# Optimization experiments

Measured on AMD Instinct MI355X. Metric: run time of the kernel, lower is better.

## Reference

```python
import jax, jax.numpy as jnp
import numpy as np

N, M, C = 262144, 1048576, 32768
ORIG, AF, NF, GH, H, NG = 200, 64, 32, 16, 128, 3


def setup_inputs() -> dict:
    key = jax.random.key(0)
    ks = jax.random.split(key, 16)
    w = lambda k, s: (jax.random.normal(k, s) * 0.02).astype(jnp.float32)
    d = {}
    d["atom_weights"] = jax.random.uniform(ks[0], (N, 1), dtype=jnp.float32)
    d["orig_atom_fea"] = jax.random.normal(ks[1], (N, ORIG), dtype=jnp.float32)
    d["nbr_fea"] = jax.random.normal(ks[2], (M, NF), dtype=jnp.float32)
    d["self_fea_idx"] = jax.random.randint(ks[3], (M,), 0, N)
    d["nbr_fea_idx"] = jax.random.randint(ks[4], (M,), 0, N)
    d["crystal_atom_idx"] = jnp.sort(jax.random.randint(ks[5], (N,), 0, C))
    d["emb_W"] = w(ks[6], (ORIG, AF)); d["emb_b"] = jnp.zeros((AF,), jnp.float32)
    d["filt_W"] = w(ks[7], (NG, 2 * AF + NF, AF)); d["filt_b"] = jnp.zeros((NG, AF), jnp.float32)
    d["core_W"] = w(ks[8], (NG, 2 * AF + NF, AF)); d["core_b"] = jnp.zeros((NG, AF), jnp.float32)
    d["bn_f_g"] = jnp.ones((NG, AF), jnp.float32); d["bn_f_b"] = jnp.zeros((NG, AF), jnp.float32)
    d["bn_c_g"] = jnp.ones((NG, AF), jnp.float32); d["bn_c_b"] = jnp.zeros((NG, AF), jnp.float32)
    d["bn_o_g"] = jnp.ones((NG, AF), jnp.float32); d["bn_o_b"] = jnp.zeros((NG, AF), jnp.float32)
    d["gate_W1"] = w(ks[9], (AF, GH)); d["gate_b1"] = jnp.zeros((GH,), jnp.float32)
    d["gate_bn_g"] = jnp.ones((GH,), jnp.float32); d["gate_bn_b"] = jnp.zeros((GH,), jnp.float32)
    d["gate_W2"] = w(ks[10], (GH, 1)); d["gate_b2"] = jnp.zeros((1,), jnp.float32)
    d["fc_W"] = w(ks[11], (AF, H)); d["fc_b"] = jnp.zeros((H,), jnp.float32)
    d["fc_bn_g"] = jnp.ones((H,), jnp.float32); d["fc_bn_b"] = jnp.zeros((H,), jnp.float32)
    d["out_W"] = w(ks[12], (H, 1)); d["out_b"] = jnp.zeros((1,), jnp.float32)
    return d


def _bn(x, g, b, eps=1e-5):
    # training-mode BatchNorm1d: batch stats over dim 0, biased variance
    return (x - x.mean(0)) / jnp.sqrt(x.var(0) + eps) * g + b


def reference(atom_weights, orig_atom_fea, nbr_fea, self_fea_idx, nbr_fea_idx, crystal_atom_idx,
              emb_W, emb_b, filt_W, filt_b, core_W, core_b,
              bn_f_g, bn_f_b, bn_c_g, bn_c_b, bn_o_g, bn_o_b,
              gate_W1, gate_b1, gate_bn_g, gate_bn_b, gate_W2, gate_b2,
              fc_W, fc_b, fc_bn_g, fc_bn_b, out_W, out_b):
    atom = orig_atom_fea @ emb_W + emb_b  # (N, AF)
    cnt = jnp.clip(jax.ops.segment_sum(jnp.ones((M,), atom.dtype), self_fea_idx, N), 1.0)
    for i in range(NG):  # message-passing layers
        total = jnp.concatenate([atom[self_fea_idx], atom[nbr_fea_idx], nbr_fea], axis=1)  # (M, 2AF+NF)
        f = jax.nn.sigmoid(_bn(total @ filt_W[i] + filt_b[i], bn_f_g[i], bn_f_b[i]))
        c = jax.nn.softplus(_bn(total @ core_W[i] + core_b[i], bn_c_g[i], bn_c_b[i]))
        mean = jax.ops.segment_sum(f * c, self_fea_idx, N) / cnt[:, None]  # scatter_mean
        atom = jax.nn.softplus(atom + _bn(mean, bn_o_g[i], bn_o_b[i]))
    # GlobalAttention pooling over crystals
    gate = jax.nn.relu(_bn(atom @ gate_W1 + gate_b1, gate_bn_g, gate_bn_b)) @ gate_W2 + gate_b2  # (N,1)
    gmax = jax.ops.segment_max(gate, crystal_atom_idx, C)
    gate = atom_weights * jnp.exp(gate - gmax[crystal_atom_idx])
    gate = gate / (jax.ops.segment_sum(gate, crystal_atom_idx, C)[crystal_atom_idx] + 1e-13)
    crys = jax.ops.segment_sum(gate * atom, crystal_atom_idx, C)  # (C, AF)
    crys = jax.nn.softplus(_bn(crys @ fc_W + fc_b, fc_bn_g, fc_bn_b))
    return crys @ out_W + out_b  # (C, 1)
```

## Files before the change

### kernel.cpp

```cpp
#include <hip/hip_runtime.h>
#include <cstdint>
#include <cstddef>

#define NATOM 262144
#define MEDGE 1048576
#define NCRY  32768

typedef __attribute__((ext_vector_type(8))) short short8v;
typedef __attribute__((ext_vector_type(4))) float f32x4;

__device__ __forceinline__ float4 ld4(const float* p){ return *reinterpret_cast<const float4*>(p); }

__device__ __forceinline__ float softplusf_(float x){
  return fmaxf(x, 0.0f) + log1pf(expf(-fabsf(x)));
}
__device__ __forceinline__ float softplus_fast(float x){
  return fmaxf(x, 0.0f) + __logf(1.0f + __expf(-fabsf(x)));
}
__device__ __forceinline__ float sigmoid_fast(float y){
  return __builtin_amdgcn_rcpf(1.0f + __expf(-y));
}

__device__ __forceinline__ unsigned short rne_bf16(float f){
  unsigned u = __float_as_uint(f);
  unsigned r = u + 0x7FFFu + ((u >> 16) & 1u);
  return (unsigned short)(r >> 16);
}
__device__ __forceinline__ float bfu(short s){
  return __uint_as_float(((unsigned)(unsigned short)s) << 16);
}

__device__ __forceinline__ unsigned fkey(float x){
  unsigned b = __float_as_uint(x);
  return (b & 0x80000000u) ? ~b : (b | 0x80000000u);
}
__device__ __forceinline__ float fkeyinv(unsigned k){
  unsigned b = (k & 0x80000000u) ? (k & 0x7fffffffu) : ~k;
  return __uint_as_float(b);
}

__device__ __forceinline__ void gll16(const void* g, void* l){
  __builtin_amdgcn_global_load_lds((const __attribute__((address_space(1))) unsigned*)g,
                                   (__attribute__((address_space(3))) unsigned*)l, 16, 0, 0);
}

#define CSB 32
__global__ __launch_bounds__(256) void colstage(const float* __restrict__ part,
                                                float* __restrict__ part2, int nb){
  int t = threadIdx.x;
  int rpb = nb / CSB;
  const float* p = part + (size_t)blockIdx.x*rpb*256 + t;
  float s = 0.f;
  #pragma unroll 4
  for (int r = 0; r < rpb; ++r) s += p[(size_t)r*256];
  part2[blockIdx.x*256 + t] = s;
}

__global__ __launch_bounds__(256) void hist_kernel(const int* __restrict__ sidx, int* __restrict__ cnti){
  for (int m = blockIdx.x*256 + threadIdx.x; m < MEDGE; m += gridDim.x*256)
    atomicAdd(&cnti[sidx[m]], 1);
}

__global__ __launch_bounds__(256) void scan1(const int* __restrict__ cnti,
                                             int* __restrict__ loc, int* __restrict__ bsum){
  __shared__ int sm[256];
  int t = threadIdx.x;
  int v = cnti[blockIdx.x*256 + t];
  sm[t] = v;
  __syncthreads();
  for (int off = 1; off < 256; off <<= 1){
    int x = (t >= off) ? sm[t-off] : 0;
    __syncthreads();
    sm[t] += x;
    __syncthreads();
  }
  loc[blockIdx.x*256 + t] = sm[t] - v;
  if (t == 255) bsum[blockIdx.x] = sm[255];
}

__global__ __launch_bounds__(256) void scan2(int* __restrict__ bsum){
  __shared__ int sm[256];
  int t = threadIdx.x;
  int v0 = bsum[t*4+0], v1 = bsum[t*4+1], v2 = bsum[t*4+2], v3 = bsum[t*4+3];
  int tot = v0+v1+v2+v3;
  sm[t] = tot;
  __syncthreads();
  for (int off = 1; off < 256; off <<= 1){
    int x = (t >= off) ? sm[t-off] : 0;
    __syncthreads();
    sm[t] += x;
    __syncthreads();
  }
  int te = sm[t] - tot;
  bsum[t*4+0] = te;
  bsum[t*4+1] = te + v0;
  bsum[t*4+2] = te + v0 + v1;
  bsum[t*4+3] = te + v0 + v1 + v2;
}

__global__ __launch_bounds__(256) void scan3(const int* __restrict__ loc, const int* __restrict__ bsum,
                                             int* __restrict__ base){
  int i = blockIdx.x*256 + threadIdx.x;
  base[i] = loc[i] + bsum[i >> 8];
}

__global__ __launch_bounds__(256) void recip_int(const int* __restrict__ cnti, float* __restrict__ recip){
  int n = blockIdx.x*256 + threadIdx.x;
  if (n < NATOM) recip[n] = 1.0f / fmaxf((float)cnti[n], 1.0f);
}

__global__ __launch_bounds__(256) void rank_kernel(const int* __restrict__ sidx, const int* __restrict__ nidx,
                                                   const int* __restrict__ base, int* __restrict__ ctr,
                                                   const short* __restrict__ nbr_h,
                                                   int* __restrict__ sidx_s, int* __restrict__ nidx_s,
                                                   short* __restrict__ feap){
  for (int m = blockIdx.x*256 + threadIdx.x; m < MEDGE; m += gridDim.x*256){
    int s = sidx[m];
    int p = base[s] + atomicAdd(&ctr[s], 1);
    sidx_s[p] = s;
    nidx_s[p] = nidx[m];
    const uint4* src = (const uint4*)(nbr_h + (size_t)m*32);
    uint4* dst = (uint4*)(feap + (size_t)p*32);
    dst[0]=src[0]; dst[1]=src[1]; dst[2]=src[2]; dst[3]=src[3];
  }
}

__global__ __launch_bounds__(256) void nbrprep(const float* __restrict__ nbr, short* __restrict__ nbr_h){
  for (size_t ch = (size_t)blockIdx.x*256 + threadIdx.x; ch < (size_t)MEDGE*32/8; ch += (size_t)gridDim.x*256){
    const float* s = nbr + ch*8;
    float4 a = ld4(s), b = ld4(s+4);
    float fv[8] = {a.x,a.y,a.z,a.w,b.x,b.y,b.z,b.w};
    unsigned w[4];
    #pragma unroll
    for (int i=0;i<4;i++)
      w[i] = (unsigned)rne_bf16(fv[2*i]) | ((unsigned)rne_bf16(fv[2*i+1]) << 16);
    *(uint4*)(nbr_h + ch*8) = make_uint4(w[0],w[1],w[2],w[3]);
  }
}

__global__ __launch_bounds__(256) void wprep_embed(const float* __restrict__ embW,
                                                   short* __restrict__ Weh, short* __restrict__ Wel){
  int idx = blockIdx.x*256 + threadIdx.x;
  if (idx >= 64*224) return;
  int k = idx % 224, c = idx / 224;
  float w = (k < 200) ? embW[(size_t)k*64 + c] : 0.0f;
  unsigned u = __float_as_uint(w);
  unsigned h = u & 0xFFFF0000u;
  Weh[idx] = (short)(h >> 16);
  Wel[idx] = (short)rne_bf16(w - __uint_as_float(h));
}

__global__ __launch_bounds__(256) void embed_mfma(const float* __restrict__ orig,
                                                  const short* __restrict__ Weh,
                                                  const short* __restrict__ Wel,
                                                  const float* __restrict__ bias,
                                                  short* __restrict__ atom_h,
                                                  short* __restrict__ atom_l){
  __shared__ uint4 ab4[3208];
  char* ab = (char*)ab4;
  int t = threadIdx.x, lane = t & 63, wid = t >> 6;
  int r16 = lane & 15, g = lane >> 4;
  int col = wid*16 + r16;

  short8v Bh[7], Bl[7];
  #pragma unroll
  for (int ks = 0; ks < 7; ks++){
    int o = col*224 + ks*32 + g*8;
    Bh[ks] = *(const short8v*)(Weh + o);
    Bl[ks] = *(const short8v*)(Wel + o);
  }
  float bv = bias[col];
  int n0 = blockIdx.x * 64;
  const char* src = (const char*)orig + (size_t)n0*800;
  #pragma unroll
  for (int i = 0; i < 13; i++){
    int j = wid + i*4;
    if (j < 50) gll16(src + j*1024 + lane*16, ab + j*1024);
  }
  __syncthreads();

  #pragma unroll
  for (int grp = 0; grp < 4; grp++){
    f32x4 acc = {bv, bv, bv, bv};
    const char* arow = ab + (grp*16 + r16)*800;
    #pragma unroll
    for (int ks = 0; ks < 7; ks++){
      short8v ah, al;
      if (ks < 6 || g == 0){
        const float* f = (const float*)(arow + ks*128 + g*32);
        float4 f0 = *(const float4*)f, f1 = *(const float4*)(f+4);
        float fv[8] = {f0.x,f0.y,f0.z,f0.w,f1.x,f1.y,f1.z,f1.w};
        unsigned hw[4], lw[4];
        #pragma unroll
        for (int p = 0; p < 4; p++){
          unsigned ua = __float_as_uint(fv[2*p]), ub = __float_as_uint(fv[2*p+1]);
          unsigned ha = ua & 0xFFFF0000u, hb = ub & 0xFFFF0000u;
          hw[p] = (ha >> 16) | hb;
          lw[p] = (unsigned)rne_bf16(fv[2*p]   - __uint_as_float(ha))
                | ((unsigned)rne_bf16(fv[2*p+1] - __uint_as_float(hb)) << 16);
        }
        ah = __builtin_bit_cast(short8v, make_uint4(hw[0],hw[1],hw[2],hw[3]));
        al = __builtin_bit_cast(short8v, make_uint4(lw[0],lw[1],lw[2],lw[3]));
      } else {
        ah = (short8v)0; al = (short8v)0;
      }
      acc = __builtin_amdgcn_mfma_f32_16x16x32_bf16(ah, Bh[ks], acc, 0, 0, 0);
      acc = __builtin_amdgcn_mfma_f32_16x16x32_bf16(al, Bh[ks], acc, 0, 0, 0);
      acc = __builtin_amdgcn_mfma_f32_16x16x32_bf16(ah, Bl[ks], acc, 0, 0, 0);
    }
    int rowb = n0 + grp*16 + g*4;
    #pragma unroll
    for (int r = 0; r < 4; r++){
      float a = acc[r];
      unsigned u = __float_as_uint(a), h = u & 0xFFFF0000u;
      size_t off = (size_t)(rowb + r)*64 + col;
      atom_h[off] = (short)(h >> 16);
      atom_l[off] = (short)rne_bf16(a - __uint_as_float(h));
    }
  }
}

__global__ __launch_bounds__(256) void wprep(const float* __restrict__ filtW, const float* __restrict__ coreW,
                                             short* __restrict__ Wth, short* __restrict__ Wtl){
  int idx = blockIdx.x*256 + threadIdx.x;
  if (idx >= 3*128*160) return;
  int k = idx % 160; int rest = idx / 160; int c = rest & 127; int layer = rest >> 7;
  float w = (c < 64) ? filtW[((size_t)layer*160 + k)*64 + c] : coreW[((size_t)layer*160 + k)*64 + (c-64)];
  unsigned u = __float_as_uint(w);
  unsigned h = u & 0xFFFF0000u;
  Wth[idx] = (short)(h >> 16);
  Wtl[idx] = (short)rne_bf16(w - __uint_as_float(h));
}

#define NT_PER_BLK 8

#define MFMA_B(A,B,ACC) ACC = __builtin_amdgcn_mfma_f32_16x16x32_bf16(A, B, ACC, 0, 0, 0)

template<int PASS>
__global__ __launch_bounds__(256) void edge_mfma(
    const short* __restrict__ atom_h, const short* __restrict__ atom_l,
    const short* __restrict__ nbr_h,
    const int* __restrict__ sidx, const int* __restrict__ nidx,
    const short* __restrict__ Wth, const short* __restrict__ Wtl,
    const float* __restrict__ bfp, const float* __restrict__ bcp,
    const float* __restrict__ scale, const float* __restrict__ shift,
    float* __restrict__ partial,
    float* __restrict__ meanacc)
{
  __shared__ uint4 xb[2][36*32];
  int t = threadIdx.x, lane = t & 63, wid = t >> 6;
  int r16 = lane & 15, g = lane >> 4;
  int colf = wid*16 + r16, colc = colf + 64;
  int el = lane & 31;

  short8v Bhf[5], Blf[5], Bhc[5], Blc[5];
  {
    const short* wfh = Wth + colf*160;
    const short* wch = Wth + colc*160;
    const short* wfl = Wtl + colf*160;
    const short* wcl = Wtl + colc*160;
    #pragma unroll
    for (int ks = 0; ks < 5; ks++){
      int o = ks*32 + g*8;
      Bhf[ks] = *(const short8v*)(wfh + o);
      Bhc[ks] = *(const short8v*)(wch + o);
      Blf[ks] = *(const short8v*)(wfl + o);
      Blc[ks] = *(const short8v*)(wcl + o);
    }
  }
  float bfv = bfp[colf], bcv = bcp[colf];
  float sf = 0.f, hf = 0.f, sc = 0.f, hc = 0.f;
  if (PASS == 1){ sf = scale[colf]; hf = shift[colf]; sc = scale[colc]; hc = shift[colc]; }
  float s0 = 0.f, q0 = 0.f, s1 = 0.f, q1 = 0.f;

  int tile0 = blockIdx.x * NT_PER_BLK;

  #define STAGE(BUF, TILE, SE, NE)                                              \
  {                                                                             \
    uint4* dst = (uint4*)(BUF);                                                 \
    int e0s_ = (TILE)*32;                                                       \
    _Pragma("unroll")                                                           \
    for (int j = wid; j < 18; j += 4){                                          \
      int c = 2*j + (lane >> 5);                                                \
      const short* src;                                                         \
      if      (c < 8)  src = atom_h + (size_t)(SE)*64 + c*8;                    \
      else if (c < 16) src = atom_h + (size_t)(NE)*64 + (c-8)*8;                \
      else if (c < 20) src = nbr_h + (size_t)(e0s_+el)*32 + (c-16)*8;           \
      else if (c < 28) src = atom_l + (size_t)(SE)*64 + (c-20)*8;               \
      else             src = atom_l + (size_t)(NE)*64 + (c-28)*8;               \
      gll16(src, dst + j*64);                                                   \
    }                                                                           \
  }

  int se, ne;
  { int e = tile0*32 + el; se = sidx[e]; ne = nidx[e]; }
  STAGE(xb[0], tile0, se, ne);
  { int e = (tile0+1)*32 + el; se = sidx[e]; ne = nidx[e]; }

  for (int tt = 0; tt < NT_PER_BLK; ++tt){
    asm volatile("s_waitcnt vmcnt(0)" ::: "memory");
    __builtin_amdgcn_s_barrier();
    if (tt+1 < NT_PER_BLK){
      STAGE(xb[(tt+1)&1], tile0+tt+1, se, ne);
      if (tt+2 < NT_PER_BLK){ int e = (tile0+tt+2)*32 + el; se = sidx[e]; ne = nidx[e]; }
    }
    int e0 = (tile0+tt)*32;
    const char* buf = (const char*)xb[tt & 1];
    #pragma unroll
    for (int grp = 0; grp < 2; ++grp){
      f32x4 accf = {bfv,bfv,bfv,bfv}, accc = {bcv,bcv,bcv,bcv};
      const char* base = buf + (grp*16 + r16)*16;
      #pragma unroll
      for (int ks = 0; ks < 5; ++ks){
        short8v ah = *(const short8v*)(base + (ks*4+g)*512);
        MFMA_B(ah, Bhf[ks], accf); MFMA_B(ah, Bhc[ks], accc);
        MFMA_B(ah, Blf[ks], accf); MFMA_B(ah, Blc[ks], accc);
        if (ks < 4){
          short8v al = *(const short8v*)(base + (20+ks*4+g)*512);
          MFMA_B(al, Bhf[ks], accf); MFMA_B(al, Bhc[ks], accc);
        }
      }
      if (PASS == 0){
        #pragma unroll
        for (int r = 0; r < 4; r++){
          float yf = accf[r], yc = accc[r];
          s0 += yf; q0 += yf*yf; s1 += yc; q1 += yc*yc;
        }
      } else {
        int ebase = e0 + grp*16 + g*4;
        int a_prev = sidx[ebase];
        float accum = 0.f;
        #pragma unroll
        for (int r = 0; r < 4; r++){
          float f  = sigmoid_fast(accf[r]*sf + hf);
          float c2 = softplus_fast(accc[r]*sc + hc);
          int a = sidx[ebase + r];
          if (a != a_prev){
            atomicAdd(&meanacc[(size_t)a_prev*64 + colf], accum);
            accum = 0.f;
            a_prev = a;
          }
          accum += f*c2;
        }
        atomicAdd(&meanacc[(size_t)a_prev*64 + colf], accum);
      }
    }
  }
  #undef STAGE

  if (PASS == 0){
    s0 += __shfl_xor(s0,16); s0 += __shfl_xor(s0,32);
    q0 += __shfl_xor(q0,16); q0 += __shfl_xor(q0,32);
    s1 += __shfl_xor(s1,16); s1 += __shfl_xor(s1,32);
    q1 += __shfl_xor(q1,16); q1 += __shfl_xor(q1,32);
    __syncthreads();
    float* scm = (float*)&xb[0][0];
    if (g == 0)
      *(float4*)&scm[(wid*16 + r16)*4] = make_float4(s0, q0, s1, q1);
    __syncthreads();
    {
      int stat = t >> 7, colx = t & 127;
      int isc = (colx >= 64) ? 1 : 0;
      int cc = colx & 63;
      int v = isc*2 + stat;
      partial[(size_t)blockIdx.x*256 + stat*128 + colx] = scm[((cc>>4)*16 + (cc&15))*4 + v];
    }
  }
}

__global__ void bnfin_kernel(int nf, float invcnt, const float* __restrict__ p2,
                             const float* __restrict__ g, const float* __restrict__ b,
                             float* __restrict__ scale, float* __restrict__ shift){
  int j = threadIdx.x;
  if (j >= nf) return;
  float s = 0.f, q = 0.f;
  #pragma unroll 4
  for (int r = 0; r < CSB; ++r){
    s += p2[r*256 + j];
    q += p2[r*256 + 128 + j];
  }
  float m = s*invcnt;
  float v = fmaxf(q*invcnt - m*m, 0.0f);
  float is = rsqrtf(v + 1e-5f);
  float sc = g[j]*is;
  scale[j] = sc;
  shift[j] = b[j] - m*sc;
}

__global__ void bnfin2_kernel(float invcnt, const float* __restrict__ p2,
                              const float* __restrict__ g0, const float* __restrict__ b0,
                              const float* __restrict__ g1, const float* __restrict__ b1,
                              float* __restrict__ scale, float* __restrict__ shift){
  int j = threadIdx.x;
  float s = 0.f, q = 0.f;
  #pragma unroll 4
  for (int r = 0; r < CSB; ++r){
    s += p2[r*256 + j];
    q += p2[r*256 + 128 + j];
  }
  float m = s*invcnt;
  float v = fmaxf(q*invcnt - m*m, 0.0f);
  float is = rsqrtf(v + 1e-5f);
  float gg = (j < 64) ? g0[j] : g1[j-64];
  float bb = (j < 64) ? b0[j] : b1[j-64];
  float sc = gg*is;
  scale[j] = sc;
  shift[j] = bb - m*sc;
}

__global__ __launch_bounds__(256) void meanbn_stats(const float* __restrict__ recip,
                                                    const float* __restrict__ meanacc,
                                                    float* __restrict__ partial){
  int t = threadIdx.x;
  float s = 0.f, q = 0.f;
  for (size_t idx = (size_t)blockIdx.x*256 + t; idx < (size_t)NATOM*64; idx += (size_t)gridDim.x*256){
    int n = (int)(idx >> 6);
    float v = meanacc[idx]*recip[n];
    s += v; q += v*v;
  }
  __shared__ float red[256][2];
  red[t][0]=s; red[t][1]=q;
  __syncthreads();
  if (t < 64){
    for (int i=1;i<4;i++){ s += red[t+64*i][0]; q += red[t+64*i][1]; }
    partial[(size_t)blockIdx.x*256 + t]       = s;
    partial[(size_t)blockIdx.x*256 + 128 + t] = q;
  }
}

__global__ __launch_bounds__(256) void atom_update(short* __restrict__ atom_h,
                                                   short* __restrict__ atom_l,
                                                   float* __restrict__ meanacc,
                                                   const float* __restrict__ recip,
                                                   const float* __restrict__ scale,
                                                   const float* __restrict__ shift){
  for (size_t idx = (size_t)blockIdx.x*256 + threadIdx.x; idx < (size_t)NATOM*64; idx += (size_t)gridDim.x*256){
    int n = (int)(idx >> 6), j = (int)(idx & 63);
    float prev = bfu(atom_h[idx]) + bfu(atom_l[idx]);
    float a = softplus_fast(prev + meanacc[idx]*recip[n]*scale[j] + shift[j]);
    meanacc[idx] = 0.0f;
    unsigned u = __float_as_uint(a), h = u & 0xFFFF0000u;
    atom_h[idx] = (short)(h >> 16);
    atom_l[idx] = (short)rne_bf16(a - __uint_as_float(h));
  }
}

__global__ __launch_bounds__(256, 2) void gate_pass1(const short* __restrict__ atom_h,
                                                     const short* __restrict__ atom_l,
                                                     const float* __restrict__ W1, const float* __restrict__ b1,
                                                     float* __restrict__ hbuf,
                                                     float* __restrict__ partial){
  __shared__ float As[256*65];
  __shared__ float Wl[64*16];
  int t = threadIdx.x;
  *(float4*)&Wl[t*4] = ld4(W1 + t*4);
  const short* hsrc = atom_h + (size_t)blockIdx.x*256*64;
  const short* lsrc = atom_l + (size_t)blockIdx.x*256*64;
  #pragma unroll
  for (int j = 0; j < 8; j++){
    int idx = j*256 + t;
    uint4 hv = *(const uint4*)(hsrc + idx*8);
    uint4 lv = *(const uint4*)(lsrc + idx*8);
    int r = idx >> 3, c = (idx & 7)*8;
    float* d = &As[r*65 + c];
    unsigned hw[4] = {hv.x,hv.y,hv.z,hv.w}, lw[4] = {lv.x,lv.y,lv.z,lv.w};
    #pragma unroll
    for (int i = 0; i < 4; i++){
      d[2*i]   = __uint_as_float(hw[i] << 16)          + __uint_as_float(lw[i] << 16);
      d[2*i+1] = __uint_as_float(hw[i] & 0xFFFF0000u)  + __uint_as_float(lw[i] & 0xFFFF0000u);
    }
  }
  __syncthreads();
  float h[16];
  #pragma unroll
  for (int c=0;c<16;c++) h[c] = b1[c];
  const float* ar = &As[t*65];
  #pragma unroll 8
  for (int k=0;k<64;k++){
    float a = ar[k];
    #pragma unroll
    for (int c=0;c<16;c++) h[c] += a*Wl[k*16+c];
  }
  size_t n = (size_t)blockIdx.x*256 + t;
  #pragma unroll
  for (int c=0;c<16;c+=4)
    *(float4*)&hbuf[n*16+c] = make_float4(h[c],h[c+1],h[c+2],h[c+3]);
  __syncthreads();
  #pragma unroll
  for (int c=0;c<16;c++){
    float v = h[c], v2 = h[c]*h[c];
    for (int off=32; off; off>>=1){ v += __shfl_down(v,off); v2 += __shfl_down(v2,off); }
    if ((t&63)==0){ As[(t>>6)*32 + c] = v; As[(t>>6)*32 + 16 + c] = v2; }
  }
  __syncthreads();
  if (t < 32){
    float v = As[t] + As[32+t] + As[64+t] + As[96+t];
    int col = (t < 16) ? t : (128 + t - 16);
    partial[(size_t)blockIdx.x*256 + col] = v;
  }
}

__global__ __launch_bounds__(256) void gate_pass2(const float* __restrict__ hbuf,
                                                  const float* __restrict__ scale, const float* __restrict__ shift,
                                                  const float* __restrict__ W2, const float* __restrict__ b2,
                                                  const int* __restrict__ cry,
                                                  float* __restrict__ gate, unsigned* __restrict__ gmaxk){
  int n = blockIdx.x*256 + threadIdx.x;
  float g = b2[0];
  #pragma unroll
  for (int c=0;c<16;c+=4){
    float4 hv = ld4(hbuf + (size_t)n*16 + c);
    float4 sc = ld4(scale + c), sh = ld4(shift + c), w = ld4(W2 + c);
    g += fmaxf(hv.x*sc.x+sh.x,0.f)*w.x + fmaxf(hv.y*sc.y+sh.y,0.f)*w.y
       + fmaxf(hv.z*sc.z+sh.z,0.f)*w.z + fmaxf(hv.w*sc.w+sh.w,0.f)*w.w;
  }
  gate[n] = g;
  atomicMax(&gmaxk[cry[n]], fkey(g));
}

__global__ __launch_bounds__(256) void gate_exp(float* __restrict__ gate,
                                                const float* __restrict__ aw,
                                                const int* __restrict__ cry,
                                                const unsigned* __restrict__ gmaxk,
                                                float* __restrict__ gsum){
  int n = blockIdx.x*256 + threadIdx.x;
  if (n < NATOM){
    int c = cry[n];
    float w = aw[n]*expf(gate[n] - fkeyinv(gmaxk[c]));
    gate[n] = w;
    atomicAdd(&gsum[c], w);
  }
}

__global__ __launch_bounds__(256) void crys_acc(const float* __restrict__ gate,
                                                const float* __restrict__ gsum,
                                                const int* __restrict__ cry,
                                                const short* __restrict__ atom_h,
                                                const short* __restrict__ atom_l,
                                                float* __restrict__ crys){
  for (size_t idx = (size_t)blockIdx.x*256 + threadIdx.x; idx < (size_t)NATOM*64; idx += (size_t)gridDim.x*256){
    int n = (int)(idx >> 6), j = (int)(idx & 63);
    int c = cry[n];
    float wn = gate[n] / (gsum[c] + 1e-13f);
    float a = bfu(atom_h[idx]) + bfu(atom_l[idx]);
    atomicAdd(&crys[(size_t)c*64 + j], wn*a);
  }
}

__global__ __launch_bounds__(512) void fc_stats(const float* __restrict__ crys,
                                                const float* __restrict__ fcW, const float* __restrict__ fcb,
                                                float* __restrict__ hid,
                                                float* __restrict__ partial){
  __shared__ float Wl[64*128];
  __shared__ float cb[64][16];
  int t = threadIdx.x;
  for (int j = t; j < 64*32; j += 512)
    *(float4*)&Wl[j*4] = ld4(fcW + j*4);
  int cg = t & 31, cr = t >> 5;
  float4 bias = ld4(fcb + cg*4);
  float ssum[4] = {0,0,0,0}, ssq[4] = {0,0,0,0};
  for (int chunk = blockIdx.x; chunk < NCRY/16; chunk += gridDim.x){
    int c0 = chunk*16;
    __syncthreads();
    for (int j = t; j < 256; j += 512){
      int rr = j & 15, c = j >> 4;
      float4 v = ld4(crys + (size_t)(c0+rr)*64 + c*4);
      int k = c*4;
      cb[k][rr]=v.x; cb[k+1][rr]=v.y; cb[k+2][rr]=v.z; cb[k+3][rr]=v.w;
    }
    __syncthreads();
    float4 acc = bias;
    #pragma unroll 4
    for (int k=0;k<64;k++){
      float a = cb[k][cr];
      float4 w = *(float4*)&Wl[k*128 + cg*4];
      acc.x += a*w.x; acc.y += a*w.y; acc.z += a*w.z; acc.w += a*w.w;
    }
    *(float4*)&hid[(size_t)(c0+cr)*128 + cg*4] = acc;
    ssum[0]+=acc.x; ssum[1]+=acc.y; ssum[2]+=acc.z; ssum[3]+=acc.w;
    ssq[0]+=acc.x*acc.x; ssq[1]+=acc.y*acc.y; ssq[2]+=acc.z*acc.z; ssq[3]+=acc.w*acc.w;
  }
  __syncthreads();
  float* red = Wl;
  #pragma unroll
  for (int q=0;q<4;q++){ red[t*8+q] = ssum[q]; red[t*8+4+q] = ssq[q]; }
  __syncthreads();
  if (t < 128){
    int cgj = t >> 2, q = t & 3;
    float s = 0.f, sq = 0.f;
    for (int cri=0; cri<16; cri++){
      int tt = cri*32 + cgj;
      s  += red[tt*8+q];
      sq += red[tt*8+4+q];
    }
    partial[(size_t)blockIdx.x*256 + t]       = s;
    partial[(size_t)blockIdx.x*256 + 128 + t] = sq;
  }
}

__global__ __launch_bounds__(256) void out_kernel(const float* __restrict__ hid,
                                                  const float* __restrict__ scale, const float* __restrict__ shift,
                                                  const float* __restrict__ outW, const float* __restrict__ outb,
                                                  float* __restrict__ out){
  int c = blockIdx.x*4 + (threadIdx.x >> 6);
  int l = threadIdx.x & 63;
  float v = softplusf_(hid[(size_t)c*128 + l]*scale[l] + shift[l])*outW[l]
          + softplusf_(hid[(size_t)c*128 + 64 + l]*scale[64+l] + shift[64+l])*outW[64+l];
  for (int off=32; off; off >>= 1) v += __shfl_down(v, off);
  if (l == 0) out[c] = v + outb[0];
}

extern "C" void kernel_launch(void* const* d_in, const int* in_sizes, int n_in,
                              void* d_out, int out_size, void* d_ws, size_t ws_size,
                              hipStream_t stream){
  const float* aw    = (const float*)d_in[0];
  const float* orig  = (const float*)d_in[1];
  const float* nbr   = (const float*)d_in[2];
  const int*   sidx  = (const int*)d_in[3];
  const int*   nidx  = (const int*)d_in[4];
  const int*   cry   = (const int*)d_in[5];
  const float* embW  = (const float*)d_in[6];
  const float* embB  = (const float*)d_in[7];
  const float* filtW = (const float*)d_in[8];
  const float* filtB = (const float*)d_in[9];
  const float* coreW = (const float*)d_in[10];
  const float* coreB = (const float*)d_in[11];
  const float* bnfg  = (const float*)d_in[12];
  const float* bnfb  = (const float*)d_in[13];
  const float* bncg  = (const float*)d_in[14];
  const float* bncb  = (const float*)d_in[15];
  const float* bnog  = (const float*)d_in[16];
  const float* bnob  = (const float*)d_in[17];
  const float* gW1   = (const float*)d_in[18];
  const float* gb1   = (const float*)d_in[19];
  const float* gbng  = (const float*)d_in[20];
  const float* gbnb  = (const float*)d_in[21];
  const float* gW2   = (const float*)d_in[22];
  const float* gb2   = (const float*)d_in[23];
  const float* fcW   = (const float*)d_in[24];
  const float* fcb   = (const float*)d_in[25];
  const float* fcbng = (const float*)d_in[26];
  const float* fcbnb = (const float*)d_in[27];
  const float* outW  = (const float*)d_in[28];
  const float* outb  = (const float*)d_in[29];
  float* out = (float*)d_out;

  float* ws      = (float*)d_ws;
  float* meanacc = ws;
  float* cnt     = meanacc + (size_t)NATOM*64;
  float* gate    = cnt     + NATOM;
  float* gmaxk   = gate    + NATOM;
  float* gsum    = gmaxk   + NCRY;
  float* crys    = gsum    + NCRY;
  float* hid     = crys    + (size_t)NCRY*64;
  float* part2   = hid     + (size_t)NCRY*128;
  float* scale   = part2   + 32*256;
  float* shift   = scale   + 128;
  short* wth     = (short*)(shift + 128);
  short* wtl     = wth + 3*128*160;
  float* partial = (float*)(wtl + 3*128*160);
  short* atom_h  = (short*)(partial + 4096*256);
  short* atom_l  = atom_h + (size_t)NATOM*64;
  short* nbr_h   = atom_l + (size_t)NATOM*64;
  short* weh     = nbr_h + (size_t)MEDGE*32;
  short* wel     = weh + 64*224;
  short* feap    = wel + 64*224;
  int*   cnti    = (int*)(feap + (size_t)MEDGE*32);
  int*   loc     = cnti + NATOM;
  int*   base    = loc + NATOM;
  int*   ctr     = base + NATOM;
  int*   bsum    = ctr + NATOM;
  int*   sidx_s  = bsum + 1024;
  int*   nidx_s  = sidx_s + MEDGE;
  (void)in_sizes; (void)n_in; (void)out_size; (void)ws_size;

  hipMemsetAsync(cnti, 0, NATOM*sizeof(int), stream);
  hipMemsetAsync(ctr, 0, NATOM*sizeof(int), stream);
  hipMemsetAsync(meanacc, 0, (size_t)NATOM*64*sizeof(float), stream);
  hist_kernel<<<2048, 256, 0, stream>>>(sidx, cnti);
  scan1<<<NATOM/256, 256, 0, stream>>>(cnti, loc, bsum);
  scan2<<<1, 256, 0, stream>>>(bsum);
  scan3<<<NATOM/256, 256, 0, stream>>>(loc, bsum, base);
  recip_int<<<NATOM/256, 256, 0, stream>>>(cnti, cnt);
  wprep<<<240, 256, 0, stream>>>(filtW, coreW, wth, wtl);
  wprep_embed<<<56, 256, 0, stream>>>(embW, weh, wel);
  nbrprep<<<2048, 256, 0, stream>>>(nbr, nbr_h);
  rank_kernel<<<2048, 256, 0, stream>>>(sidx, nidx, base, ctr, nbr_h, sidx_s, nidx_s, feap);
  embed_mfma<<<NATOM/64, 256, 0, stream>>>(orig, weh, wel, embB, atom_h, atom_l);

  for (int i = 0; i < 3; ++i){
    const short* wthL = wth + (size_t)i*128*160;
    const short* wtlL = wtl + (size_t)i*128*160;
    const float* bf = filtB + i*64;
    const float* bc = coreB + i*64;
    edge_mfma<0><<<4096, 256, 0, stream>>>(atom_h, atom_l, feap, sidx_s, nidx_s, wthL, wtlL, bf, bc,
                                           nullptr, nullptr, partial, nullptr);
    colstage<<<CSB, 256, 0, stream>>>(partial, part2, 4096);
    bnfin2_kernel<<<1, 128, 0, stream>>>(1.0f/MEDGE, part2,
                                         bnfg+i*64, bnfb+i*64, bncg+i*64, bncb+i*64, scale, shift);
    edge_mfma<1><<<4096, 256, 0, stream>>>(atom_h, atom_l, feap, sidx_s, nidx_s, wthL, wtlL, bf, bc,
                                           scale, shift, nullptr, meanacc);
    meanbn_stats<<<2048, 256, 0, stream>>>(cnt, meanacc, partial);
    colstage<<<CSB, 256, 0, stream>>>(partial, part2, 2048);
    bnfin_kernel<<<1, 64, 0, stream>>>(64, 1.0f/NATOM, part2, bnog+i*64, bnob+i*64, scale, shift);
    atom_update<<<2048, 256, 0, stream>>>(atom_h, atom_l, meanacc, cnt, scale, shift);
  }

  float* hbuf = meanacc;
  gate_pass1<<<NATOM/256, 256, 0, stream>>>(atom_h, atom_l, gW1, gb1, hbuf, partial);
  colstage<<<CSB, 256, 0, stream>>>(partial, part2, NATOM/256);
  bnfin_kernel<<<1, 16, 0, stream>>>(16, 1.0f/NATOM, part2, gbng, gbnb, scale, shift);
  hipMemsetAsync(gmaxk, 0, NCRY*sizeof(unsigned), stream);
  gate_pass2<<<NATOM/256, 256, 0, stream>>>(hbuf, scale, shift, gW2, gb2, cry, gate, (unsigned*)gmaxk);
  hipMemsetAsync(gsum, 0, NCRY*sizeof(float), stream);
  gate_exp<<<NATOM/256, 256, 0, stream>>>(gate, aw, cry, (const unsigned*)gmaxk, gsum);
  hipMemsetAsync(crys, 0, (size_t)NCRY*64*sizeof(float), stream);
  crys_acc<<<4096, 256, 0, stream>>>(gate, gsum, cry, atom_h, atom_l, crys);

  fc_stats<<<1024, 512, 0, stream>>>(crys, fcW, fcb, hid, partial);
  colstage<<<CSB, 256, 0, stream>>>(partial, part2, 1024);
  bnfin_kernel<<<1, 128, 0, stream>>>(128, 1.0f/NCRY, part2, fcbng, fcbnb, scale, shift);
  out_kernel<<<NCRY/4, 256, 0, stream>>>(hid, scale, shift, outW, outb, out);
}
```

Measured before the change: 1.650 ms.

## Cache fp16 edge pre-activations to skip second MFMA pass; fuse nbr conversion into rank

The stats pass of the edge kernel now writes its filter and core pre-activations as fp16 into a workspace cache, and a new lightweight edge_actv kernel applies BN, the activations and the scatter-add from that cache instead of recomputing the gather and GEMM in a second edge_mfma pass. The nbr_fea bf16 conversion is also folded into rank_kernel, which removes one kernel and one intermediate buffer. The cache costs 256MB of workspace writes and reads per layer in exchange for the gather plus MFMA work, and storing pre-activations in fp16 loses some precision. The cache path runs only when the workspace is large enough; otherwise the original second pass is used.

```diff
diff --git a/kernel.cpp b/kernel.cpp
--- a/kernel.cpp
+++ b/kernel.cpp
@@ -1,4 +1,5 @@
 #include <hip/hip_runtime.h>
+#include <hip/hip_fp16.h>
 #include <cstdint>
 #include <cstddef>
 
@@ -111,7 +112,7 @@
 
 __global__ __launch_bounds__(256) void rank_kernel(const int* __restrict__ sidx, const int* __restrict__ nidx,
                                                    const int* __restrict__ base, int* __restrict__ ctr,
-                                                   const short* __restrict__ nbr_h,
+                                                   const float* __restrict__ nbr,
                                                    int* __restrict__ sidx_s, int* __restrict__ nidx_s,
                                                    short* __restrict__ feap){
   for (int m = blockIdx.x*256 + threadIdx.x; m < MEDGE; m += gridDim.x*256){
@@ -119,22 +120,18 @@
     int p = base[s] + atomicAdd(&ctr[s], 1);
     sidx_s[p] = s;
     nidx_s[p] = nidx[m];
-    const uint4* src = (const uint4*)(nbr_h + (size_t)m*32);
+    const float* src = nbr + (size_t)m*32;
     uint4* dst = (uint4*)(feap + (size_t)p*32);
-    dst[0]=src[0]; dst[1]=src[1]; dst[2]=src[2]; dst[3]=src[3];
-  }
-}
-
-__global__ __launch_bounds__(256) void nbrprep(const float* __restrict__ nbr, short* __restrict__ nbr_h){
-  for (size_t ch = (size_t)blockIdx.x*256 + threadIdx.x; ch < (size_t)MEDGE*32/8; ch += (size_t)gridDim.x*256){
-    const float* s = nbr + ch*8;
-    float4 a = ld4(s), b = ld4(s+4);
-    float fv[8] = {a.x,a.y,a.z,a.w,b.x,b.y,b.z,b.w};
-    unsigned w[4];
     #pragma unroll
-    for (int i=0;i<4;i++)
-      w[i] = (unsigned)rne_bf16(fv[2*i]) | ((unsigned)rne_bf16(fv[2*i+1]) << 16);
-    *(uint4*)(nbr_h + ch*8) = make_uint4(w[0],w[1],w[2],w[3]);
+    for (int c = 0; c < 4; ++c){
+      float4 a = ld4(src + c*8), b = ld4(src + c*8 + 4);
+      float fv[8] = {a.x,a.y,a.z,a.w,b.x,b.y,b.z,b.w};
+      unsigned w[4];
+      #pragma unroll
+      for (int i=0;i<4;i++)
+        w[i] = (unsigned)rne_bf16(fv[2*i]) | ((unsigned)rne_bf16(fv[2*i+1]) << 16);
+      dst[c] = make_uint4(w[0],w[1],w[2],w[3]);
+    }
   }
 }
 
@@ -245,7 +242,8 @@
     const float* __restrict__ bfp, const float* __restrict__ bcp,
     const float* __restrict__ scale, const float* __restrict__ shift,
     float* __restrict__ partial,
-    float* __restrict__ meanacc)
+    float* __restrict__ meanacc,
+    unsigned short* __restrict__ ycache)
 {
   __shared__ uint4 xb[2][36*32];
   int t = threadIdx.x, lane = t & 63, wid = t >> 6;
@@ -326,6 +324,18 @@
           float yf = accf[r], yc = accc[r];
           s0 += yf; q0 += yf*yf; s1 += yc; q1 += yc*yc;
         }
+        if (ycache){
+          int ebase = e0 + grp*16 + g*4;
+          uint2 pf, pc;
+          #pragma unroll
+          for (int r = 0; r < 4; r++){
+            ((__half*)&pf)[r] = __float2half_rn(accf[r]);
+            ((__half*)&pc)[r] = __float2half_rn(accc[r]);
+          }
+          uint2* yrow = (uint2*)ycache + (size_t)(ebase >> 2)*128;
+          yrow[colf]      = pf;
+          yrow[64 + colf] = pc;
+        }
       } else {
         int ebase = e0 + grp*16 + g*4;
         int a_prev = sidx[ebase];
@@ -365,6 +375,40 @@
       int v = isc*2 + stat;
       partial[(size_t)blockIdx.x*256 + stat*128 + colx] = scm[((cc>>4)*16 + (cc&15))*4 + v];
     }
+  }
+}
+
+__global__ __launch_bounds__(256) void edge_actv(const unsigned short* __restrict__ ycache,
+                                                 const int* __restrict__ sidx_s,
+                                                 const float* __restrict__ scale,
+                                                 const float* __restrict__ shift,
+                                                 float* __restrict__ meanacc){
+  int j = threadIdx.x & 63;
+  int q = threadIdx.x >> 6;
+  float sf = scale[j], hf = shift[j];
+  float sc = scale[j+64], hc = shift[j+64];
+  for (int eq = blockIdx.x*4 + q; eq < MEDGE/4; eq += gridDim.x*4){
+    const uint2* yrow = (const uint2*)ycache + (size_t)eq*128;
+    uint2 f4 = yrow[j];
+    uint2 c4 = yrow[64 + j];
+    const int* sp = sidx_s + eq*4;
+    int a_prev = sp[0];
+    float accum = 0.f;
+    #pragma unroll
+    for (int r = 0; r < 4; ++r){
+      float yf = __half2float(((const __half*)&f4)[r]);
+      float yc = __half2float(((const __half*)&c4)[r]);
+      float f  = sigmoid_fast(yf*sf + hf);
+      float c2 = softplus_fast(yc*sc + hc);
+      int a = sp[r];
+      if (a != a_prev){
+        atomicAdd(&meanacc[(size_t)a_prev*64 + j], accum);
+        accum = 0.f;
+        a_prev = a;
+      }
+      accum += f*c2;
+    }
+    atomicAdd(&meanacc[(size_t)a_prev*64 + j], accum);
   }
 }
 
@@ -661,8 +705,7 @@
   float* partial = (float*)(wtl + 3*128*160);
   short* atom_h  = (short*)(partial + 4096*256);
   short* atom_l  = atom_h + (size_t)NATOM*64;
-  short* nbr_h   = atom_l + (size_t)NATOM*64;
-  short* weh     = nbr_h + (size_t)MEDGE*32;
+  short* weh     = atom_l + (size_t)NATOM*64;
   short* wel     = weh + 64*224;
   short* feap    = wel + 64*224;
   int*   cnti    = (int*)(feap + (size_t)MEDGE*32);
@@ -672,7 +715,11 @@
   int*   bsum    = ctr + NATOM;
   int*   sidx_s  = bsum + 1024;
   int*   nidx_s  = sidx_s + MEDGE;
-  (void)in_sizes; (void)n_in; (void)out_size; (void)ws_size;
+  unsigned short* ycache = (unsigned short*)(nidx_s + MEDGE);
+  size_t need = (size_t)((char*)(ycache + (size_t)MEDGE*128) - (char*)d_ws);
+  bool use_yc = (ws_size >= need);
+  unsigned short* yc = use_yc ? ycache : nullptr;
+  (void)in_sizes; (void)n_in; (void)out_size;
 
   hipMemsetAsync(cnti, 0, NATOM*sizeof(int), stream);
   hipMemsetAsync(ctr, 0, NATOM*sizeof(int), stream);
@@ -684,8 +731,7 @@
   recip_int<<<NATOM/256, 256, 0, stream>>>(cnti, cnt);
   wprep<<<240, 256, 0, stream>>>(filtW, coreW, wth, wtl);
   wprep_embed<<<56, 256, 0, stream>>>(embW, weh, wel);
-  nbrprep<<<2048, 256, 0, stream>>>(nbr, nbr_h);
-  rank_kernel<<<2048, 256, 0, stream>>>(sidx, nidx, base, ctr, nbr_h, sidx_s, nidx_s, feap);
+  rank_kernel<<<2048, 256, 0, stream>>>(sidx, nidx, base, ctr, nbr, sidx_s, nidx_s, feap);
   embed_mfma<<<NATOM/64, 256, 0, stream>>>(orig, weh, wel, embB, atom_h, atom_l);
 
   for (int i = 0; i < 3; ++i){
@@ -694,12 +740,16 @@
     const float* bf = filtB + i*64;
     const float* bc = coreB + i*64;
     edge_mfma<0><<<4096, 256, 0, stream>>>(atom_h, atom_l, feap, sidx_s, nidx_s, wthL, wtlL, bf, bc,
-                                           nullptr, nullptr, partial, nullptr);
+                                           nullptr, nullptr, partial, nullptr, yc);
     colstage<<<CSB, 256, 0, stream>>>(partial, part2, 4096);
     bnfin2_kernel<<<1, 128, 0, stream>>>(1.0f/MEDGE, part2,
                                          bnfg+i*64, bnfb+i*64, bncg+i*64, bncb+i*64, scale, shift);
-    edge_mfma<1><<<4096, 256, 0, stream>>>(atom_h, atom_l, feap, sidx_s, nidx_s, wthL, wtlL, bf, bc,
-                                           scale, shift, nullptr, meanacc);
+    if (use_yc){
+      edge_actv<<<2048, 256, 0, stream>>>(ycache, sidx_s, scale, shift, meanacc);
+    } else {
+      edge_mfma<1><<<4096, 256, 0, stream>>>(atom_h, atom_l, feap, sidx_s, nidx_s, wthL, wtlL, bf, bc,
+                                             scale, shift, nullptr, meanacc, nullptr);
+    }
     meanbn_stats<<<2048, 256, 0, stream>>>(cnt, meanacc, partial);
     colstage<<<CSB, 256, 0, stream>>>(partial, part2, 2048);
     bnfin_kernel<<<1, 64, 0, stream>>>(64, 1.0f/NATOM, part2, bnog+i*64, bnob+i*64, scale, shift);
```

Result: faster. 1.434 ms (-13.1%).
